# Kernel optimization log

Measured on AMD Instinct MI355X. Metric: run time of the kernel, lower is better.

Reference implementation:

```python
import jax, jax.numpy as jnp
import numpy as np


def setup_inputs() -> dict:
    key = jax.random.key(0)
    kx, ky = jax.random.split(key)
    x = jax.random.normal(kx, (4096, 256), dtype=jnp.float32)
    y = jax.random.normal(ky, (16384, 256), dtype=jnp.float32)
    return {"x": x, "y": y}


def reference(x, y):
    # Original module: scan over rows of x; for each row x_i compute
    #   sqrt(sum((y - x_i)**2, axis=1))  -> stacked to [Nx, Ny].
    # Batched equivalent (single fused pass, no serial scan):
    #   ||x_i - y_j||^2 = ||x_i||^2 + ||y_j||^2 - 2 <x_i, y_j>
    x2 = jnp.sum(x * x, axis=1)                       # [Nx]
    y2 = jnp.sum(y * y, axis=1)                       # [Ny]
    xy = jnp.einsum("nd,md->nm", x, y)               # [Nx, Ny]
    d2 = x2[:, None] + y2[None, :] - 2.0 * xy
    return jnp.sqrt(jnp.maximum(d2, 0.0))            # [Nx, Ny]
```

## Files before the change

### kernel.cpp

```cpp
#include <hip/hip_runtime.h>
#include <hip/hip_bf16.h>


using bf16x8  = __attribute__((ext_vector_type(8))) short;
using f32x4   = __attribute__((ext_vector_type(4))) float;
using ushort8 = __attribute__((ext_vector_type(8))) unsigned short;

constexpr int NXR = 4096;
constexpr int NYR = 16384;
constexpr int DD  = 256;

constexpr int BM = 128;
constexpr int BN = 128;
constexpr int BK = 128;
constexpr int PK = BK + 8;

__device__ inline unsigned short f2bf(float f) {
    unsigned int b = __float_as_uint(f);
    b += 0x7FFFu + ((b >> 16) & 1u);
    return (unsigned short)(b >> 16);
}

__global__ __launch_bounds__(256) void norms_kernel(const float* __restrict__ x,
                                                    const float* __restrict__ y,
                                                    float* __restrict__ ws) {
    const int row  = blockIdx.x * 4 + (threadIdx.x >> 6);
    const int lane = threadIdx.x & 63;
    const float* src = (row < NXR) ? (x + (size_t)row * DD)
                                   : (y + (size_t)(row - NXR) * DD);
    float4 v = *(const float4*)(src + lane * 4);
    float s = v.x * v.x + v.y * v.y + v.z * v.z + v.w * v.w;
    #pragma unroll
    for (int off = 32; off > 0; off >>= 1) s += __shfl_down(s, off, 64);
    if (lane == 0) ws[row] = s;
}

__global__ __launch_bounds__(512) void dist_kernel(const float* __restrict__ x,
                                                   const float* __restrict__ y,
                                                   const float* __restrict__ xn,
                                                   const float* __restrict__ yn,
                                                   float* __restrict__ out) {
    __shared__ unsigned short lA[BM * PK];
    __shared__ unsigned short lB[BN * PK];

    const int bm = blockIdx.x;
    const int bn = blockIdx.y;
    const int tid  = threadIdx.x;
    const int wave = tid >> 6;
    const int lane = tid & 63;
    const int wm   = wave & 1;
    const int wn   = wave >> 1;
    const int quad = lane >> 4;
    const int l15  = lane & 15;

    f32x4 acc[4][2];
    #pragma unroll
    for (int i = 0; i < 4; ++i)
        #pragma unroll
        for (int j = 0; j < 2; ++j)
            acc[i][j] = f32x4{0.f, 0.f, 0.f, 0.f};

    const int sc  = (tid & 15) * 8;
    const int sr0 = tid >> 4;

    #pragma unroll
    for (int kt = 0; kt < 2; ++kt) {
        if (kt) __syncthreads();
        #pragma unroll
        for (int p = 0; p < 4; ++p) {
            const int r = p * 32 + sr0;
            const float* sa = x + (size_t)(bm * BM + r) * DD + kt * BK + sc;
            float4 a0 = *(const float4*)sa;
            float4 a1 = *(const float4*)(sa + 4);
            ushort8 ua = { f2bf(a0.x), f2bf(a0.y), f2bf(a0.z), f2bf(a0.w),
                           f2bf(a1.x), f2bf(a1.y), f2bf(a1.z), f2bf(a1.w) };
            *(ushort8*)&lA[r * PK + sc] = ua;
            const float* sb = y + (size_t)(bn * BN + r) * DD + kt * BK + sc;
            float4 b0 = *(const float4*)sb;
            float4 b1 = *(const float4*)(sb + 4);
            ushort8 ub = { f2bf(b0.x), f2bf(b0.y), f2bf(b0.z), f2bf(b0.w),
                           f2bf(b1.x), f2bf(b1.y), f2bf(b1.z), f2bf(b1.w) };
            *(ushort8*)&lB[r * PK + sc] = ub;
        }
        __syncthreads();
        const int ar = (wm * 64 + l15) * PK;
        const int br = (wn * 32 + l15) * PK;
        #pragma unroll
        for (int kk = 0; kk < 4; ++kk) {
            const int k = kk * 32 + quad * 8;
            bf16x8 av[4], bv[2];
            #pragma unroll
            for (int i = 0; i < 4; ++i)
                av[i] = *(const bf16x8*)&lA[ar + i * 16 * PK + k];
            #pragma unroll
            for (int j = 0; j < 2; ++j)
                bv[j] = *(const bf16x8*)&lB[br + j * 16 * PK + k];
            #pragma unroll
            for (int i = 0; i < 4; ++i)
                #pragma unroll
                for (int j = 0; j < 2; ++j)
                    acc[i][j] = __builtin_amdgcn_mfma_f32_16x16x32_bf16(
                        av[i], bv[j], acc[i][j], 0, 0, 0);
        }
    }

    const int gr_base = bm * BM + wm * 64;
    const int gc_base = bn * BN + wn * 32;
    #pragma unroll
    for (int i = 0; i < 4; ++i) {
        const int gr0 = gr_base + i * 16 + quad * 4;
        #pragma unroll
        for (int r = 0; r < 4; ++r) {
            const float xv = xn[gr0 + r];
            const size_t ro = (size_t)(gr0 + r) * NYR;
            #pragma unroll
            for (int j = 0; j < 2; ++j) {
                const int gc = gc_base + j * 16 + l15;
                const float d2 = xv + yn[gc] - 2.0f * acc[i][j][r];
                out[ro + gc] = sqrtf(fmaxf(d2, 0.0f));
            }
        }
    }
}

extern "C" void kernel_launch(void* const* d_in, const int* in_sizes, int n_in,
                              void* d_out, int out_size, void* d_ws, size_t ws_size,
                              hipStream_t stream) {
    const float* x = (const float*)d_in[0];
    const float* y = (const float*)d_in[1];
    float* ws  = (float*)d_ws;
    float* out = (float*)d_out;

    norms_kernel<<<(NXR + NYR) / 4, 256, 0, stream>>>(x, y, ws);
    dist_kernel<<<dim3(NXR / BM, NYR / BN), 512, 0, stream>>>(x, y, ws, ws + NXR, out);
}
```

Baseline: 339.0 us.

## Pre-convert inputs to bf16 and stream tiles via direct global-to-LDS loads

The prep kernel now writes bf16 copies of x and y alongside the norms. The distance kernel loads 64-wide K tiles straight into swizzled LDS with global_load_lds, instead of converting fp32 in registers. It also uses 4 waves with 64x64 warp tiles and remaps block IDs so each XCD shares x row-tiles. The aim is to halve global reads in the GEMM and cut conversion and LDS-store overhead, at the cost of an extra bf16 workspace write and more accumulator registers.

```diff
diff --git a/kernel.cpp b/kernel.cpp
--- a/kernel.cpp
+++ b/kernel.cpp
@@ -1,10 +1,9 @@
 #include <hip/hip_runtime.h>
-#include <hip/hip_bf16.h>
 
 
-using bf16x8  = __attribute__((ext_vector_type(8))) short;
-using f32x4   = __attribute__((ext_vector_type(4))) float;
-using ushort8 = __attribute__((ext_vector_type(8))) unsigned short;
+using bf16x8   = __attribute__((ext_vector_type(8))) short;
+using f32x4    = __attribute__((ext_vector_type(4))) float;
+using ushort4v = __attribute__((ext_vector_type(4))) unsigned short;
 
 constexpr int NXR = 4096;
 constexpr int NYR = 16384;
@@ -12,8 +11,7 @@
 
 constexpr int BM = 128;
 constexpr int BN = 128;
-constexpr int BK = 128;
-constexpr int PK = BK + 8;
+constexpr int BK = 64;
 
 __device__ inline unsigned short f2bf(float f) {
     unsigned int b = __float_as_uint(f);
@@ -21,30 +19,53 @@
     return (unsigned short)(b >> 16);
 }
 
-__global__ __launch_bounds__(256) void norms_kernel(const float* __restrict__ x,
-                                                    const float* __restrict__ y,
-                                                    float* __restrict__ ws) {
+__device__ inline void gl_lds16(const void* g, void* l) {
+    __builtin_amdgcn_global_load_lds(
+        (const __attribute__((address_space(1))) void*)g,
+        (__attribute__((address_space(3))) void*)l, 16, 0, 0);
+}
+
+__global__ __launch_bounds__(256) void prep_kernel(const float* __restrict__ x,
+                                                   const float* __restrict__ y,
+                                                   float* __restrict__ ws) {
+    float* xn = ws;
+    float* yn = ws + NXR;
+    unsigned short* xb = (unsigned short*)(ws + NXR + NYR);
+    unsigned short* yb = xb + (size_t)NXR * DD;
+
     const int row  = blockIdx.x * 4 + (threadIdx.x >> 6);
     const int lane = threadIdx.x & 63;
-    const float* src = (row < NXR) ? (x + (size_t)row * DD)
-                                   : (y + (size_t)(row - NXR) * DD);
+    const bool isx = row < NXR;
+    const int  r   = isx ? row : row - NXR;
+    const float* src        = (isx ? x  : y ) + (size_t)r * DD;
+    unsigned short* dst     = (isx ? xb : yb) + (size_t)r * DD;
+
     float4 v = *(const float4*)(src + lane * 4);
+    ushort4v b = { f2bf(v.x), f2bf(v.y), f2bf(v.z), f2bf(v.w) };
+    *(ushort4v*)(dst + lane * 4) = b;
+
     float s = v.x * v.x + v.y * v.y + v.z * v.z + v.w * v.w;
     #pragma unroll
     for (int off = 32; off > 0; off >>= 1) s += __shfl_down(s, off, 64);
-    if (lane == 0) ws[row] = s;
+    if (lane == 0) (isx ? xn : yn)[r] = s;
 }
 
-__global__ __launch_bounds__(512) void dist_kernel(const float* __restrict__ x,
-                                                   const float* __restrict__ y,
-                                                   const float* __restrict__ xn,
-                                                   const float* __restrict__ yn,
+__global__ __launch_bounds__(256) void dist_kernel(const float* __restrict__ ws,
                                                    float* __restrict__ out) {
-    __shared__ unsigned short lA[BM * PK];
-    __shared__ unsigned short lB[BN * PK];
+    __shared__ unsigned short lA[BM * BK];
+    __shared__ unsigned short lB[BN * BK];
 
-    const int bm = blockIdx.x;
-    const int bn = blockIdx.y;
+    const float* xn = ws;
+    const float* yn = ws + NXR;
+    const unsigned short* xb = (const unsigned short*)(ws + NXR + NYR);
+    const unsigned short* yb = xb + (size_t)NXR * DD;
+
+    const int bid = blockIdx.x;
+    const int xcd = bid & 7;
+    const int loc = bid >> 3;
+    const int bm  = xcd * 4 + (loc & 3);
+    const int bn  = loc >> 2;
+
     const int tid  = threadIdx.x;
     const int wave = tid >> 6;
     const int lane = tid & 63;
@@ -53,71 +74,66 @@
     const int quad = lane >> 4;
     const int l15  = lane & 15;
 
-    f32x4 acc[4][2];
+    const int rl = lane >> 3;
+    const int sl = (lane & 7) ^ rl;
+    const unsigned short* ag = xb + (size_t)(bm * BM + wave * 32 + rl) * DD + sl * 8;
+    const unsigned short* bg = yb + (size_t)(bn * BN + wave * 32 + rl) * DD + sl * 8;
+
+    f32x4 acc[4][4];
     #pragma unroll
     for (int i = 0; i < 4; ++i)
         #pragma unroll
-        for (int j = 0; j < 2; ++j)
+        for (int j = 0; j < 4; ++j)
             acc[i][j] = f32x4{0.f, 0.f, 0.f, 0.f};
 
-    const int sc  = (tid & 15) * 8;
-    const int sr0 = tid >> 4;
+    const int arow = wm * 64 + l15;
+    const int brow = wn * 64 + l15;
+    const int s7   = l15 & 7;
 
     #pragma unroll
-    for (int kt = 0; kt < 2; ++kt) {
+    for (int kt = 0; kt < 4; ++kt) {
         if (kt) __syncthreads();
         #pragma unroll
-        for (int p = 0; p < 4; ++p) {
-            const int r = p * 32 + sr0;
-            const float* sa = x + (size_t)(bm * BM + r) * DD + kt * BK + sc;
-            float4 a0 = *(const float4*)sa;
-            float4 a1 = *(const float4*)(sa + 4);
-            ushort8 ua = { f2bf(a0.x), f2bf(a0.y), f2bf(a0.z), f2bf(a0.w),
-                           f2bf(a1.x), f2bf(a1.y), f2bf(a1.z), f2bf(a1.w) };
-            *(ushort8*)&lA[r * PK + sc] = ua;
-            const float* sb = y + (size_t)(bn * BN + r) * DD + kt * BK + sc;
-            float4 b0 = *(const float4*)sb;
-            float4 b1 = *(const float4*)(sb + 4);
-            ushort8 ub = { f2bf(b0.x), f2bf(b0.y), f2bf(b0.z), f2bf(b0.w),
-                           f2bf(b1.x), f2bf(b1.y), f2bf(b1.z), f2bf(b1.w) };
-            *(ushort8*)&lB[r * PK + sc] = ub;
+        for (int q = 0; q < 4; ++q) {
+            gl_lds16(ag + (size_t)q * 8 * DD + kt * BK, &lA[(wave * 4 + q) * 512]);
+            gl_lds16(bg + (size_t)q * 8 * DD + kt * BK, &lB[(wave * 4 + q) * 512]);
         }
         __syncthreads();
-        const int ar = (wm * 64 + l15) * PK;
-        const int br = (wn * 32 + l15) * PK;
         #pragma unroll
-        for (int kk = 0; kk < 4; ++kk) {
-            const int k = kk * 32 + quad * 8;
-            bf16x8 av[4], bv[2];
+        for (int kk = 0; kk < 2; ++kk) {
+            const int ka = (((kk << 2) | quad) ^ s7) << 3;
+            bf16x8 av[4], bv[4];
             #pragma unroll
             for (int i = 0; i < 4; ++i)
-                av[i] = *(const bf16x8*)&lA[ar + i * 16 * PK + k];
+                av[i] = *(const bf16x8*)&lA[(arow + i * 16) * BK + ka];
             #pragma unroll
-            for (int j = 0; j < 2; ++j)
-                bv[j] = *(const bf16x8*)&lB[br + j * 16 * PK + k];
+            for (int j = 0; j < 4; ++j)
+                bv[j] = *(const bf16x8*)&lB[(brow + j * 16) * BK + ka];
             #pragma unroll
             for (int i = 0; i < 4; ++i)
                 #pragma unroll
-                for (int j = 0; j < 2; ++j)
+                for (int j = 0; j < 4; ++j)
                     acc[i][j] = __builtin_amdgcn_mfma_f32_16x16x32_bf16(
                         av[i], bv[j], acc[i][j], 0, 0, 0);
         }
     }
 
     const int gr_base = bm * BM + wm * 64;
-    const int gc_base = bn * BN + wn * 32;
+    const int gc_base = bn * BN + wn * 64;
+    float ynv[4];
+    #pragma unroll
+    for (int j = 0; j < 4; ++j) ynv[j] = yn[gc_base + j * 16 + l15];
     #pragma unroll
     for (int i = 0; i < 4; ++i) {
         const int gr0 = gr_base + i * 16 + quad * 4;
         #pragma unroll
         for (int r = 0; r < 4; ++r) {
             const float xv = xn[gr0 + r];
-            const size_t ro = (size_t)(gr0 + r) * NYR;
+            float* op = out + (size_t)(gr0 + r) * NYR + gc_base;
             #pragma unroll
-            for (int j = 0; j < 2; ++j) {
-                const int gc = gc_base + j * 16 + l15;
-                const float d2 = xv + yn[gc] - 2.0f * acc[i][j][r];
-                out[ro + gc] = sqrtf(fmaxf(d2, 0.0f));
+            for (int j = 0; j < 4; ++j) {
+                const float d2 = xv + ynv[j] - 2.0f * acc[i][j][r];
+                op[j * 16 + l15] = sqrtf(fmaxf(d2, 0.0f));
             }
         }
     }
@@ -131,6 +147,6 @@
     float* ws  = (float*)d_ws;
     float* out = (float*)d_out;
 
-    norms_kernel<<<(NXR + NYR) / 4, 256, 0, stream>>>(x, y, ws);
-    dist_kernel<<<dim3(NXR / BM, NYR / BN), 512, 0, stream>>>(x, y, ws, ws + NXR, out);
+    prep_kernel<<<(NXR + NYR) / 4, 256, 0, stream>>>(x, y, ws);
+    dist_kernel<<<(NXR / BM) * (NYR / BN), 256, 0, stream>>>(ws, out);
 }
```

Measured after the change: 321.0 us. -5.3%, faster.
